# Performance work log

Hardware: AMD Instinct MI355X
Metric: run time of the kernel (lower is better)

Reference implementation:

```python
import jax, jax.numpy as jnp
import numpy as np

UP_FACTOR = 8
POINT_ORDER_WEIGHT = 0.1


def _interp_linear(x, size):
    """torch.nn.functional.interpolate(mode='linear', align_corners=True) on last dim.
    x: (N, C, W) -> (N, C, size)"""
    W = x.shape[-1]
    pos = jnp.linspace(0.0, W - 1.0, size)          # align_corners=True mapping
    i0 = jnp.floor(pos).astype(jnp.int32)
    i1 = jnp.minimum(i0 + 1, W - 1)
    w = (pos - i0.astype(pos.dtype)).astype(x.dtype)
    return x[..., i0] * (1.0 - w) + x[..., i1] * w


def _directed_loss(points1, points2, mask):
    """Chamfer-style directed loss: for each point in points2, min sq-dist to points1,
    plus index-order penalty on the argmin indices. points*: (N, 2, W')."""
    # pairwise sq distances: d[n, i, j] = sum_c (points2[n,c,i] - points1[n,c,j])^2
    d = jnp.square(points2[:, :, :, None] - points1[:, :, None, :]).sum(axis=1)  # (N, W', W')
    mse_error = d.min(axis=2)                         # (N, W')
    indices = d.argmin(axis=2)                        # (N, W') int
    neg_index_diffs = -(indices[:, 1:] - indices[:, :-1]).astype(jnp.float32)
    neg_index_diffs = jnp.square(jax.nn.relu(neg_index_diffs))
    mse_error = mse_error * mask
    neg_index_diffs = neg_index_diffs * mask[:, :-1]
    return mse_error.mean() + (POINT_ORDER_WEIGHT * neg_index_diffs).mean()


def setup_inputs() -> dict:
    key = jax.random.key(0)
    k1, k2, k3 = jax.random.split(key, 3)
    N, C, W = 128, 2, 128
    return {
        "target_points": jax.random.normal(k1, (N, C, W), dtype=jnp.float32),
        "predictions": jax.random.normal(k2, (N, C, W), dtype=jnp.float32),
        "visibility_mask": jax.random.uniform(k3, (N, W), dtype=jnp.float32),
    }


def reference(target_points, predictions, visibility_mask):
    size = target_points.shape[2] * UP_FACTOR  # compared_size = W * up_factor
    t = _interp_linear(target_points, size)    # (N, 2, W')
    p = _interp_linear(predictions, size)      # (N, 2, W')
    m = _interp_linear(visibility_mask[:, None, :], size)[:, 0, :]  # (N, W')
    m = jnp.where(m < 0.5, jnp.zeros_like(m), m)

    # direct (aligned) error
    error_direct = (jnp.square(t - p).sum(axis=1) * m).mean(axis=1)  # (N,)

    # symmetric matched (chamfer + index-order) error
    error_matched = 0.5 * _directed_loss(p, t, m) + 0.5 * _directed_loss(t, p, m)

    return jnp.minimum(error_matched, error_direct.mean())
```

## Files before the change

kernel.cpp:

```cpp
#include <hip/hip_runtime.h>

#define N_BATCH 128
#define W_RAW   128
#define NSEG    (W_RAW - 1)
#define W_UP    1024
#define TPB     256
#define QCHUNK  4
#define QPB     256
#define SCHUNK  4
#define SPC     32
#define NBLK    (N_BATCH * 2 * QCHUNK)

#define WS_S 0
#define WS_P 1024
#define WS_D 2048
#define WS_I 3072

__device__ __forceinline__ void interp_setup(int i, int& i0, int& i1, float& w, float& w0) {
    const double step = 127.0 / 1023.0;
    double pos = (double)i * step;
    i0 = (int)pos;
    if (i0 > W_RAW - 1) i0 = W_RAW - 1;
    i1 = min(i0 + 1, W_RAW - 1);
    w  = (float)(pos - (double)i0);
    w0 = __fsub_rn(1.0f, w);
}

__global__ __launch_bounds__(TPB) void chamfer_kernel(
    const float* __restrict__ tp,
    const float* __restrict__ pr,
    const float* __restrict__ vm,
    float* __restrict__ ws)
{
    __shared__ float2 s_c[W_UP];
    __shared__ float4 s_segA[NSEG];
    __shared__ float2 s_segB[NSEG];
    __shared__ float  s_pd[SCHUNK][QPB];
    __shared__ int    s_pi[SCHUNK][QPB];
    __shared__ float  s_red[4 * 3];

    const int bid    = blockIdx.x;
    const int qchunk = bid & (QCHUNK - 1);
    const int dir    = (bid >> 2) & 1;
    const int n      = bid >> 3;
    const int tid    = threadIdx.x;
    const int nd     = n * 2 + dir;

    const float* q_base = (dir == 0) ? tp : pr;
    const float* c_base = (dir == 0) ? pr : tp;
    const float* qx_raw = q_base + (size_t)(n * 2 + 0) * W_RAW;
    const float* qy_raw = q_base + (size_t)(n * 2 + 1) * W_RAW;
    const float* cx_raw = c_base + (size_t)(n * 2 + 0) * W_RAW;
    const float* cy_raw = c_base + (size_t)(n * 2 + 1) * W_RAW;
    const float* m_raw  = vm + (size_t)n * W_RAW;

    #pragma unroll
    for (int k = 0; k < W_UP / TPB; ++k) {
        const int i = tid + k * TPB;
        int i0, i1; float w, w0;
        interp_setup(i, i0, i1, w, w0);
        const float cx = __fadd_rn(__fmul_rn(cx_raw[i0], w0), __fmul_rn(cx_raw[i1], w));
        const float cy = __fadd_rn(__fmul_rn(cy_raw[i0], w0), __fmul_rn(cy_raw[i1], w));
        s_c[i] = make_float2(cx, cy);
    }

    if (tid < NSEG) {
        const int s = tid;
        const float ax = cx_raw[s],     ay = cy_raw[s];
        const float bx = cx_raw[s + 1], by = cy_raw[s + 1];
        const float abx = bx - ax, aby = by - ay;
        const float len2 = abx * abx + aby * aby;
        const float inv  = (len2 > 0.0f) ? (1.0f / len2) : 0.0f;
        const float Kx = abx * inv, Ky = aby * inv;
        const float bb = -(ax * abx + ay * aby) * inv;
        const float s8h = (float)s * (1023.0f / 127.0f) + 0.5f;
        s_segA[s] = make_float4(Kx, Ky, bb, s8h);
        s_segB[s] = make_float2((float)((s * 1023 + 126) / 127),
                                (float)(((s + 1) * 1023) / 127));
    }

    const int jc = tid >> 6;
    const int g  = tid & 63;

    float qx[4], qy[4];
    #pragma unroll
    for (int k = 0; k < 4; ++k) {
        const int qi = qchunk * QPB + g * 4 + k;
        int i0, i1; float w, w0;
        interp_setup(qi, i0, i1, w, w0);
        qx[k] = __fadd_rn(__fmul_rn(qx_raw[i0], w0), __fmul_rn(qx_raw[i1], w));
        qy[k] = __fadd_rn(__fmul_rn(qy_raw[i0], w0), __fmul_rn(qy_raw[i1], w));
    }
    __syncthreads();

    float bestd[4];
    int   bidx[4];
    #pragma unroll
    for (int k = 0; k < 4; ++k) { bestd[k] = 3.4e38f; bidx[k] = 0; }

    const int sbase = jc * SPC;
    const int send  = min(sbase + SPC, NSEG);
    #pragma unroll 4
    for (int s = sbase; s < send; ++s) {
        const float4 SA = s_segA[s];
        const float2 SB = s_segB[s];
        #pragma unroll
        for (int k = 0; k < 4; ++k) {
            const float t  = __builtin_fmaf(qy[k], SA.y, __builtin_fmaf(qx[k], SA.x, SA.z));
            float ic = __builtin_fmaf(t, 1023.0f / 127.0f, SA.w);
            ic = fminf(fmaxf(ic, SB.x), SB.y);
            const int i0 = (int)ic;
            const float2 c0 = s_c[i0];
            const float dx0 = __fsub_rn(qx[k], c0.x);
            const float dy0 = __fsub_rn(qy[k], c0.y);
            const float d0  = __fadd_rn(__fmul_rn(dx0, dx0), __fmul_rn(dy0, dy0));
            const bool lt = d0 < bestd[k];
            bestd[k] = lt ? d0 : bestd[k];
            bidx[k]  = lt ? i0 : bidx[k];
        }
    }

    #pragma unroll
    for (int k = 0; k < 4; ++k) {
        const int q = g * 4 + k;
        s_pd[jc][q] = bestd[k];
        s_pi[jc][q] = bidx[k];
    }
    __syncthreads();

    float bd = s_pd[0][tid];
    int   bi = s_pi[0][tid];
    #pragma unroll
    for (int c = 1; c < SCHUNK; ++c) {
        const float d2 = s_pd[c][tid];
        const bool lt = d2 < bd;
        bd = lt ? d2 : bd;
        bi = lt ? s_pi[c][tid] : bi;
    }
    s_pi[0][tid] = bi;

    const int qi = qchunk * QPB + tid;
    ((int*)(ws + WS_I))[(size_t)nd * W_UP + qi] = bi;

    int i0m, i1m; float wm, w0m;
    interp_setup(qi, i0m, i1m, wm, w0m);
    const float qxm = __fadd_rn(__fmul_rn(qx_raw[i0m], w0m), __fmul_rn(qx_raw[i1m], wm));
    const float qym = __fadd_rn(__fmul_rn(qy_raw[i0m], w0m), __fmul_rn(qy_raw[i1m], wm));
    const float mv  = __fadd_rn(__fmul_rn(m_raw[i0m], w0m), __fmul_rn(m_raw[i1m], wm));
    const float mq  = (mv < 0.5f) ? 0.0f : mv;

    float S = bd * mq;
    float D = 0.0f;
    if (dir == 0) {
        const float2 c = s_c[qi];
        const float dx = qxm - c.x;
        const float dy = qym - c.y;
        D = (dx * dx + dy * dy) * mq;
    }
    __syncthreads();

    float P = 0.0f;
    if (tid < QPB - 1) {
        const float df = (float)(s_pi[0][tid] - s_pi[0][tid + 1]);
        const float r  = fmaxf(df, 0.0f);
        P = r * r * mq;
    }

    #pragma unroll
    for (int off = 32; off > 0; off >>= 1) {
        S += __shfl_down(S, off, 64);
        P += __shfl_down(P, off, 64);
        D += __shfl_down(D, off, 64);
    }
    const int wave = tid >> 6, lane = tid & 63;
    if (lane == 0) {
        s_red[wave * 3 + 0] = S;
        s_red[wave * 3 + 1] = P;
        s_red[wave * 3 + 2] = D;
    }
    __syncthreads();
    if (tid == 0) {
        float St = 0.f, Pt = 0.f, Dt = 0.f;
        #pragma unroll
        for (int w2 = 0; w2 < TPB / 64; ++w2) {
            St += s_red[w2 * 3 + 0];
            Pt += s_red[w2 * 3 + 1];
            Dt += s_red[w2 * 3 + 2];
        }
        ws[WS_S + bid] = St;
        ws[WS_P + bid] = Pt;
        ws[WS_D + bid] = Dt;
    }
}

__global__ __launch_bounds__(TPB) void finalize_kernel(
    const float* __restrict__ vm,
    const float* __restrict__ ws,
    float* __restrict__ out)
{
    __shared__ float s_red[4 * 3];
    const int tid = threadIdx.x;

    float S = 0.f, P = 0.f, D = 0.f;
    #pragma unroll
    for (int k = 0; k < NBLK / TPB; ++k) {
        const int b = tid + k * TPB;
        S += ws[WS_S + b];
        P += ws[WS_P + b];
        D += ws[WS_D + b];
    }

    if (tid < N_BATCH * 2 * (QCHUNK - 1)) {
        const int nd = tid / (QCHUNK - 1);
        const int b  = tid % (QCHUNK - 1) + 1;
        const int i  = b * QPB - 1;
        const int n  = nd >> 1;
        const int* widx = (const int*)(ws + WS_I) + (size_t)nd * W_UP;
        const float df = (float)(widx[i] - widx[i + 1]);
        const float r  = fmaxf(df, 0.0f);
        int i0, i1; float w, w0;
        interp_setup(i, i0, i1, w, w0);
        const float* m_raw = vm + (size_t)n * W_RAW;
        float mv = __fadd_rn(__fmul_rn(m_raw[i0], w0), __fmul_rn(m_raw[i1], w));
        const float mq = (mv < 0.5f) ? 0.0f : mv;
        P += r * r * mq;
    }

    #pragma unroll
    for (int off = 32; off > 0; off >>= 1) {
        S += __shfl_down(S, off, 64);
        P += __shfl_down(P, off, 64);
        D += __shfl_down(D, off, 64);
    }
    const int wave = tid >> 6, lane = tid & 63;
    if (lane == 0) {
        s_red[wave * 3 + 0] = S;
        s_red[wave * 3 + 1] = P;
        s_red[wave * 3 + 2] = D;
    }
    __syncthreads();
    if (tid == 0) {
        float St = 0.f, Pt = 0.f, Dt = 0.f;
        #pragma unroll
        for (int w2 = 0; w2 < TPB / 64; ++w2) {
            St += s_red[w2 * 3 + 0];
            Pt += s_red[w2 * 3 + 1];
            Dt += s_red[w2 * 3 + 2];
        }
        const float nw  = (float)(N_BATCH * W_UP);
        const float nw1 = (float)(N_BATCH * (W_UP - 1));
        const float matched = St / (2.0f * nw) + 0.1f * Pt / (2.0f * nw1);
        const float direct  = Dt / nw;
        out[0] = fminf(matched, direct);
    }
}

extern "C" void kernel_launch(void* const* d_in, const int* in_sizes, int n_in,
                              void* d_out, int out_size, void* d_ws, size_t ws_size,
                              hipStream_t stream) {
    const float* tp = (const float*)d_in[0];
    const float* pr = (const float*)d_in[1];
    const float* vm = (const float*)d_in[2];
    float* out = (float*)d_out;
    float* ws  = (float*)d_ws;

    chamfer_kernel<<<NBLK, TPB, 0, stream>>>(tp, pr, vm, ws);
    finalize_kernel<<<1, TPB, 0, stream>>>(vm, ws, out);
}
```

Measured before the change: 73.98 us.

## Split queries into 8 chunks per direction and store only chunk boundary indices

Doubles the number of blocks by halving queries per block (128 instead of 256), so each thread handles 2 queries instead of 4, which spreads work over more CUs. Instead of writing all argmin indices to the workspace, each block stores only the first and last index of its chunk, and the finalize kernel now loops over the larger set of chunk boundaries. It also adds a launch-bounds occupancy hint. The trade-off is that every block redundantly rebuilds the upsampled candidate curve and segment tables, and half the threads sit idle during the final per-query reduction.

```diff
diff --git a/kernel.cpp b/kernel.cpp
--- a/kernel.cpp
+++ b/kernel.cpp
@@ -5,16 +5,16 @@
 #define NSEG    (W_RAW - 1)
 #define W_UP    1024
 #define TPB     256
-#define QCHUNK  4
-#define QPB     256
+#define QCHUNK  8
+#define QPB     128
 #define SCHUNK  4
 #define SPC     32
 #define NBLK    (N_BATCH * 2 * QCHUNK)
 
 #define WS_S 0
-#define WS_P 1024
-#define WS_D 2048
-#define WS_I 3072
+#define WS_P NBLK
+#define WS_D (2 * NBLK)
+#define WS_I (3 * NBLK)
 
 __device__ __forceinline__ void interp_setup(int i, int& i0, int& i1, float& w, float& w0) {
     const double step = 127.0 / 1023.0;
@@ -26,7 +26,7 @@
     w0 = __fsub_rn(1.0f, w);
 }
 
-__global__ __launch_bounds__(TPB) void chamfer_kernel(
+__global__ __launch_bounds__(TPB, 8) void chamfer_kernel(
     const float* __restrict__ tp,
     const float* __restrict__ pr,
     const float* __restrict__ vm,
@@ -41,8 +41,8 @@
 
     const int bid    = blockIdx.x;
     const int qchunk = bid & (QCHUNK - 1);
-    const int dir    = (bid >> 2) & 1;
-    const int n      = bid >> 3;
+    const int dir    = (bid >> 3) & 1;
+    const int n      = bid >> 4;
     const int tid    = threadIdx.x;
     const int nd     = n * 2 + dir;
 
@@ -82,10 +82,10 @@
     const int jc = tid >> 6;
     const int g  = tid & 63;
 
-    float qx[4], qy[4];
-    #pragma unroll
-    for (int k = 0; k < 4; ++k) {
-        const int qi = qchunk * QPB + g * 4 + k;
+    float qx[2], qy[2];
+    #pragma unroll
+    for (int k = 0; k < 2; ++k) {
+        const int qi = qchunk * QPB + g * 2 + k;
         int i0, i1; float w, w0;
         interp_setup(qi, i0, i1, w, w0);
         qx[k] = __fadd_rn(__fmul_rn(qx_raw[i0], w0), __fmul_rn(qx_raw[i1], w));
@@ -93,10 +93,10 @@
     }
     __syncthreads();
 
-    float bestd[4];
-    int   bidx[4];
-    #pragma unroll
-    for (int k = 0; k < 4; ++k) { bestd[k] = 3.4e38f; bidx[k] = 0; }
+    float bestd[2];
+    int   bidx[2];
+    #pragma unroll
+    for (int k = 0; k < 2; ++k) { bestd[k] = 3.4e38f; bidx[k] = 0; }
 
     const int sbase = jc * SPC;
     const int send  = min(sbase + SPC, NSEG);
@@ -105,7 +105,7 @@
         const float4 SA = s_segA[s];
         const float2 SB = s_segB[s];
         #pragma unroll
-        for (int k = 0; k < 4; ++k) {
+        for (int k = 0; k < 2; ++k) {
             const float t  = __builtin_fmaf(qy[k], SA.y, __builtin_fmaf(qx[k], SA.x, SA.z));
             float ic = __builtin_fmaf(t, 1023.0f / 127.0f, SA.w);
             ic = fminf(fmaxf(ic, SB.x), SB.y);
@@ -121,45 +121,49 @@
     }
 
     #pragma unroll
-    for (int k = 0; k < 4; ++k) {
-        const int q = g * 4 + k;
+    for (int k = 0; k < 2; ++k) {
+        const int q = g * 2 + k;
         s_pd[jc][q] = bestd[k];
         s_pi[jc][q] = bidx[k];
     }
     __syncthreads();
 
-    float bd = s_pd[0][tid];
-    int   bi = s_pi[0][tid];
-    #pragma unroll
-    for (int c = 1; c < SCHUNK; ++c) {
-        const float d2 = s_pd[c][tid];
-        const bool lt = d2 < bd;
-        bd = lt ? d2 : bd;
-        bi = lt ? s_pi[c][tid] : bi;
-    }
-    s_pi[0][tid] = bi;
-
-    const int qi = qchunk * QPB + tid;
-    ((int*)(ws + WS_I))[(size_t)nd * W_UP + qi] = bi;
-
-    int i0m, i1m; float wm, w0m;
-    interp_setup(qi, i0m, i1m, wm, w0m);
-    const float qxm = __fadd_rn(__fmul_rn(qx_raw[i0m], w0m), __fmul_rn(qx_raw[i1m], wm));
-    const float qym = __fadd_rn(__fmul_rn(qy_raw[i0m], w0m), __fmul_rn(qy_raw[i1m], wm));
-    const float mv  = __fadd_rn(__fmul_rn(m_raw[i0m], w0m), __fmul_rn(m_raw[i1m], wm));
-    const float mq  = (mv < 0.5f) ? 0.0f : mv;
-
-    float S = bd * mq;
-    float D = 0.0f;
-    if (dir == 0) {
-        const float2 c = s_c[qi];
-        const float dx = qxm - c.x;
-        const float dy = qym - c.y;
-        D = (dx * dx + dy * dy) * mq;
-    }
-    __syncthreads();
-
-    float P = 0.0f;
+    float S = 0.0f, P = 0.0f, D = 0.0f;
+    float mq = 0.0f;
+    int   bi = 0;
+    if (tid < QPB) {
+        float bd = s_pd[0][tid];
+        bi = s_pi[0][tid];
+        #pragma unroll
+        for (int c = 1; c < SCHUNK; ++c) {
+            const float d2 = s_pd[c][tid];
+            const bool lt = d2 < bd;
+            bd = lt ? d2 : bd;
+            bi = lt ? s_pi[c][tid] : bi;
+        }
+        s_pi[0][tid] = bi;
+
+        const int qi = qchunk * QPB + tid;
+
+        int i0m, i1m; float wm, w0m;
+        interp_setup(qi, i0m, i1m, wm, w0m);
+        const float qxm = __fadd_rn(__fmul_rn(qx_raw[i0m], w0m), __fmul_rn(qx_raw[i1m], wm));
+        const float qym = __fadd_rn(__fmul_rn(qy_raw[i0m], w0m), __fmul_rn(qy_raw[i1m], wm));
+        const float mv  = __fadd_rn(__fmul_rn(m_raw[i0m], w0m), __fmul_rn(m_raw[i1m], wm));
+        mq = (mv < 0.5f) ? 0.0f : mv;
+
+        S = bd * mq;
+        if (dir == 0) {
+            const float2 c = s_c[qi];
+            const float dx = qxm - c.x;
+            const float dy = qym - c.y;
+            D = (dx * dx + dy * dy) * mq;
+        }
+    }
+    if (tid == 0)       ((int*)(ws + WS_I))[nd * 16 + qchunk * 2 + 0] = bi;
+    if (tid == QPB - 1) ((int*)(ws + WS_I))[nd * 16 + qchunk * 2 + 1] = bi;
+    __syncthreads();
+
     if (tid < QPB - 1) {
         const float df = (float)(s_pi[0][tid] - s_pi[0][tid + 1]);
         const float r  = fmaxf(df, 0.0f);
@@ -210,13 +214,15 @@
         D += ws[WS_D + b];
     }
 
-    if (tid < N_BATCH * 2 * (QCHUNK - 1)) {
-        const int nd = tid / (QCHUNK - 1);
-        const int b  = tid % (QCHUNK - 1) + 1;
+    const int* wsI = (const int*)(ws + WS_I);
+    for (int e = tid; e < N_BATCH * 2 * (QCHUNK - 1); e += TPB) {
+        const int nd = e / (QCHUNK - 1);
+        const int b  = e % (QCHUNK - 1) + 1;
         const int i  = b * QPB - 1;
         const int n  = nd >> 1;
-        const int* widx = (const int*)(ws + WS_I) + (size_t)nd * W_UP;
-        const float df = (float)(widx[i] - widx[i + 1]);
+        const int idx_last  = wsI[nd * 16 + (b - 1) * 2 + 1];
+        const int idx_first = wsI[nd * 16 + b * 2 + 0];
+        const float df = (float)(idx_last - idx_first);
         const float r  = fmaxf(df, 0.0f);
         int i0, i1; float w, w0;
         interp_setup(i, i0, i1, w, w0);
```

Measured after the change: 75.54 us. 1.02x slower.

## Split interpolation and segment setup into a prep kernel, one query per thread

Applied to the files above, without the earlier changes.

Adds a prep kernel that interpolates points and mask once and precomputes per-segment projection coefficients into workspace, replacing the per-block recomputation that was repeated across the four query chunks and two directions. The chamfer kernel now loads those precomputed arrays. Each thread handles one query over all 127 segments, which removes the cross-wave partial-min reduction through shared memory. Only the boundary argmin indices are written out for the finalize step. The cost is an extra kernel launch and global round trip, plus segment data read from global memory with uniform addresses instead of from LDS.

```diff
diff --git a/kernel.cpp b/kernel.cpp
--- a/kernel.cpp
+++ b/kernel.cpp
@@ -7,14 +7,17 @@
 #define TPB     256
 #define QCHUNK  4
 #define QPB     256
-#define SCHUNK  4
-#define SPC     32
 #define NBLK    (N_BATCH * 2 * QCHUNK)
 
-#define WS_S 0
-#define WS_P 1024
-#define WS_D 2048
-#define WS_I 3072
+#define WS_S  0
+#define WS_P  1024
+#define WS_D  2048
+#define WS_I  3072
+#define WS_T  8192
+#define WS_PP (WS_T + 2 * 128 * 1024)
+#define WS_M  (WS_PP + 2 * 128 * 1024)
+#define WS_GA (WS_M + 128 * 1024)
+#define WS_GB (WS_GA + 2 * 128 * NSEG * 4)
 
 __device__ __forceinline__ void interp_setup(int i, int& i0, int& i1, float& w, float& w0) {
     const double step = 127.0 / 1023.0;
@@ -26,17 +29,68 @@
     w0 = __fsub_rn(1.0f, w);
 }
 
-__global__ __launch_bounds__(TPB) void chamfer_kernel(
+__global__ __launch_bounds__(TPB) void prep_kernel(
     const float* __restrict__ tp,
     const float* __restrict__ pr,
     const float* __restrict__ vm,
     float* __restrict__ ws)
 {
+    const int b   = blockIdx.x;
+    const int tid = threadIdx.x;
+
+    if (b < 256) {
+        const int which = b >> 7;
+        const int n     = b & 127;
+        const float* src   = (which == 0) ? tp : pr;
+        const float* x_raw = src + (size_t)(n * 2 + 0) * W_RAW;
+        const float* y_raw = src + (size_t)(n * 2 + 1) * W_RAW;
+        float2* dst = (float2*)(ws + (which == 0 ? WS_T : WS_PP)) + (size_t)n * W_UP;
+
+        #pragma unroll
+        for (int k = 0; k < W_UP / TPB; ++k) {
+            const int i = tid + k * TPB;
+            int i0, i1; float w, w0;
+            interp_setup(i, i0, i1, w, w0);
+            const float cx = __fadd_rn(__fmul_rn(x_raw[i0], w0), __fmul_rn(x_raw[i1], w));
+            const float cy = __fadd_rn(__fmul_rn(y_raw[i0], w0), __fmul_rn(y_raw[i1], w));
+            dst[i] = make_float2(cx, cy);
+        }
+
+        if (tid < NSEG) {
+            const int s = tid;
+            const float ax = x_raw[s],     ay = y_raw[s];
+            const float bx = x_raw[s + 1], by = y_raw[s + 1];
+            const float abx = bx - ax, aby = by - ay;
+            const float len2 = abx * abx + aby * aby;
+            const float inv  = (len2 > 0.0f) ? (1.0f / len2) : 0.0f;
+            const float Kx = abx * inv, Ky = aby * inv;
+            const float bb = -(ax * abx + ay * aby) * inv;
+            const float s8h = (float)s * (1023.0f / 127.0f) + 0.5f;
+            ((float4*)(ws + WS_GA))[(size_t)(which * 128 + n) * NSEG + s] =
+                make_float4(Kx, Ky, bb, s8h);
+            ((float2*)(ws + WS_GB))[(size_t)(which * 128 + n) * NSEG + s] =
+                make_float2((float)((s * 1023 + 126) / 127),
+                            (float)(((s + 1) * 1023) / 127));
+        }
+    } else {
+        const int n = b - 256;
+        const float* m_raw = vm + (size_t)n * W_RAW;
+        float* dst = ws + WS_M + (size_t)n * W_UP;
+        #pragma unroll
+        for (int k = 0; k < W_UP / TPB; ++k) {
+            const int i = tid + k * TPB;
+            int i0, i1; float w, w0;
+            interp_setup(i, i0, i1, w, w0);
+            dst[i] = __fadd_rn(__fmul_rn(m_raw[i0], w0), __fmul_rn(m_raw[i1], w));
+        }
+    }
+}
+
+__global__ __launch_bounds__(TPB) void chamfer_kernel(
+    float* __restrict__ ws)
+{
     __shared__ float2 s_c[W_UP];
-    __shared__ float4 s_segA[NSEG];
-    __shared__ float2 s_segB[NSEG];
-    __shared__ float  s_pd[SCHUNK][QPB];
-    __shared__ int    s_pi[SCHUNK][QPB];
+    __shared__ int    s_pi[QPB];
     __shared__ float  s_red[4 * 3];
 
     const int bid    = blockIdx.x;
@@ -46,122 +100,62 @@
     const int tid    = threadIdx.x;
     const int nd     = n * 2 + dir;
 
-    const float* q_base = (dir == 0) ? tp : pr;
-    const float* c_base = (dir == 0) ? pr : tp;
-    const float* qx_raw = q_base + (size_t)(n * 2 + 0) * W_RAW;
-    const float* qy_raw = q_base + (size_t)(n * 2 + 1) * W_RAW;
-    const float* cx_raw = c_base + (size_t)(n * 2 + 0) * W_RAW;
-    const float* cy_raw = c_base + (size_t)(n * 2 + 1) * W_RAW;
-    const float* m_raw  = vm + (size_t)n * W_RAW;
-
-    #pragma unroll
-    for (int k = 0; k < W_UP / TPB; ++k) {
-        const int i = tid + k * TPB;
-        int i0, i1; float w, w0;
-        interp_setup(i, i0, i1, w, w0);
-        const float cx = __fadd_rn(__fmul_rn(cx_raw[i0], w0), __fmul_rn(cx_raw[i1], w));
-        const float cy = __fadd_rn(__fmul_rn(cy_raw[i0], w0), __fmul_rn(cy_raw[i1], w));
-        s_c[i] = make_float2(cx, cy);
-    }
-
-    if (tid < NSEG) {
-        const int s = tid;
-        const float ax = cx_raw[s],     ay = cy_raw[s];
-        const float bx = cx_raw[s + 1], by = cy_raw[s + 1];
-        const float abx = bx - ax, aby = by - ay;
-        const float len2 = abx * abx + aby * aby;
-        const float inv  = (len2 > 0.0f) ? (1.0f / len2) : 0.0f;
-        const float Kx = abx * inv, Ky = aby * inv;
-        const float bb = -(ax * abx + ay * aby) * inv;
-        const float s8h = (float)s * (1023.0f / 127.0f) + 0.5f;
-        s_segA[s] = make_float4(Kx, Ky, bb, s8h);
-        s_segB[s] = make_float2((float)((s * 1023 + 126) / 127),
-                                (float)(((s + 1) * 1023) / 127));
-    }
-
-    const int jc = tid >> 6;
-    const int g  = tid & 63;
-
-    float qx[4], qy[4];
-    #pragma unroll
-    for (int k = 0; k < 4; ++k) {
-        const int qi = qchunk * QPB + g * 4 + k;
-        int i0, i1; float w, w0;
-        interp_setup(qi, i0, i1, w, w0);
-        qx[k] = __fadd_rn(__fmul_rn(qx_raw[i0], w0), __fmul_rn(qx_raw[i1], w));
-        qy[k] = __fadd_rn(__fmul_rn(qy_raw[i0], w0), __fmul_rn(qy_raw[i1], w));
-    }
-    __syncthreads();
-
-    float bestd[4];
-    int   bidx[4];
-    #pragma unroll
-    for (int k = 0; k < 4; ++k) { bestd[k] = 3.4e38f; bidx[k] = 0; }
-
-    const int sbase = jc * SPC;
-    const int send  = min(sbase + SPC, NSEG);
+    const int cw = (dir == 0) ? 1 : 0;
+    const float2* ccur = (const float2*)(ws + (cw ? WS_PP : WS_T)) + (size_t)n * W_UP;
+    const float2* qcur = (const float2*)(ws + (cw ? WS_T : WS_PP)) + (size_t)n * W_UP;
+    const float4* gA   = (const float4*)(ws + WS_GA) + (size_t)(cw * 128 + n) * NSEG;
+    const float2* gB   = (const float2*)(ws + WS_GB) + (size_t)(cw * 128 + n) * NSEG;
+
+    {
+        const float4* c4  = (const float4*)ccur;
+        float4*       s4  = (float4*)s_c;
+        s4[tid]       = c4[tid];
+        s4[tid + TPB] = c4[tid + TPB];
+    }
+
+    const int qi = qchunk * QPB + tid;
+    const float2 q  = qcur[qi];
+    const float  mv = ws[WS_M + (size_t)n * W_UP + qi];
+    const float  mq = (mv < 0.5f) ? 0.0f : mv;
+    __syncthreads();
+
+    float bd = 3.4e38f;
+    int   bi = 0;
     #pragma unroll 4
-    for (int s = sbase; s < send; ++s) {
-        const float4 SA = s_segA[s];
-        const float2 SB = s_segB[s];
-        #pragma unroll
-        for (int k = 0; k < 4; ++k) {
-            const float t  = __builtin_fmaf(qy[k], SA.y, __builtin_fmaf(qx[k], SA.x, SA.z));
-            float ic = __builtin_fmaf(t, 1023.0f / 127.0f, SA.w);
-            ic = fminf(fmaxf(ic, SB.x), SB.y);
-            const int i0 = (int)ic;
-            const float2 c0 = s_c[i0];
-            const float dx0 = __fsub_rn(qx[k], c0.x);
-            const float dy0 = __fsub_rn(qy[k], c0.y);
-            const float d0  = __fadd_rn(__fmul_rn(dx0, dx0), __fmul_rn(dy0, dy0));
-            const bool lt = d0 < bestd[k];
-            bestd[k] = lt ? d0 : bestd[k];
-            bidx[k]  = lt ? i0 : bidx[k];
-        }
-    }
-
-    #pragma unroll
-    for (int k = 0; k < 4; ++k) {
-        const int q = g * 4 + k;
-        s_pd[jc][q] = bestd[k];
-        s_pi[jc][q] = bidx[k];
-    }
-    __syncthreads();
-
-    float bd = s_pd[0][tid];
-    int   bi = s_pi[0][tid];
-    #pragma unroll
-    for (int c = 1; c < SCHUNK; ++c) {
-        const float d2 = s_pd[c][tid];
-        const bool lt = d2 < bd;
-        bd = lt ? d2 : bd;
-        bi = lt ? s_pi[c][tid] : bi;
-    }
-    s_pi[0][tid] = bi;
-
-    const int qi = qchunk * QPB + tid;
-    ((int*)(ws + WS_I))[(size_t)nd * W_UP + qi] = bi;
-
-    int i0m, i1m; float wm, w0m;
-    interp_setup(qi, i0m, i1m, wm, w0m);
-    const float qxm = __fadd_rn(__fmul_rn(qx_raw[i0m], w0m), __fmul_rn(qx_raw[i1m], wm));
-    const float qym = __fadd_rn(__fmul_rn(qy_raw[i0m], w0m), __fmul_rn(qy_raw[i1m], wm));
-    const float mv  = __fadd_rn(__fmul_rn(m_raw[i0m], w0m), __fmul_rn(m_raw[i1m], wm));
-    const float mq  = (mv < 0.5f) ? 0.0f : mv;
+    for (int s = 0; s < NSEG; ++s) {
+        const float4 SA = gA[s];
+        const float2 SB = gB[s];
+        const float t  = __builtin_fmaf(q.y, SA.y, __builtin_fmaf(q.x, SA.x, SA.z));
+        float ic = __builtin_fmaf(t, 1023.0f / 127.0f, SA.w);
+        ic = fminf(fmaxf(ic, SB.x), SB.y);
+        const int i0 = (int)ic;
+        const float2 c0 = s_c[i0];
+        const float dx0 = __fsub_rn(q.x, c0.x);
+        const float dy0 = __fsub_rn(q.y, c0.y);
+        const float d0  = __fadd_rn(__fmul_rn(dx0, dx0), __fmul_rn(dy0, dy0));
+        const bool lt = d0 < bd;
+        bd = lt ? d0 : bd;
+        bi = lt ? i0 : bi;
+    }
+
+    s_pi[tid] = bi;
+
+    if (tid == 0)       ((int*)(ws + WS_I))[nd * 8 + qchunk * 2 + 0] = bi;
+    if (tid == QPB - 1) ((int*)(ws + WS_I))[nd * 8 + qchunk * 2 + 1] = bi;
 
     float S = bd * mq;
     float D = 0.0f;
     if (dir == 0) {
         const float2 c = s_c[qi];
-        const float dx = qxm - c.x;
-        const float dy = qym - c.y;
+        const float dx = q.x - c.x;
+        const float dy = q.y - c.y;
         D = (dx * dx + dy * dy) * mq;
     }
     __syncthreads();
 
     float P = 0.0f;
     if (tid < QPB - 1) {
-        const float df = (float)(s_pi[0][tid] - s_pi[0][tid + 1]);
+        const float df = (float)(s_pi[tid] - s_pi[tid + 1]);
         const float r  = fmaxf(df, 0.0f);
         P = r * r * mq;
     }
@@ -194,7 +188,6 @@
 }
 
 __global__ __launch_bounds__(TPB) void finalize_kernel(
-    const float* __restrict__ vm,
     const float* __restrict__ ws,
     float* __restrict__ out)
 {
@@ -210,18 +203,17 @@
         D += ws[WS_D + b];
     }
 
-    if (tid < N_BATCH * 2 * (QCHUNK - 1)) {
-        const int nd = tid / (QCHUNK - 1);
-        const int b  = tid % (QCHUNK - 1) + 1;
-        const int i  = b * QPB - 1;
-        const int n  = nd >> 1;
-        const int* widx = (const int*)(ws + WS_I) + (size_t)nd * W_UP;
-        const float df = (float)(widx[i] - widx[i + 1]);
+    const int* wsI = (const int*)(ws + WS_I);
+    for (int e = tid; e < N_BATCH * 2 * (QCHUNK - 1); e += TPB) {
+        const int ndb = e / (QCHUNK - 1);
+        const int b   = e % (QCHUNK - 1) + 1;
+        const int i   = b * QPB - 1;
+        const int nn  = ndb >> 1;
+        const int idx_last  = wsI[ndb * 8 + (b - 1) * 2 + 1];
+        const int idx_first = wsI[ndb * 8 + b * 2 + 0];
+        const float df = (float)(idx_last - idx_first);
         const float r  = fmaxf(df, 0.0f);
-        int i0, i1; float w, w0;
-        interp_setup(i, i0, i1, w, w0);
-        const float* m_raw = vm + (size_t)n * W_RAW;
-        float mv = __fadd_rn(__fmul_rn(m_raw[i0], w0), __fmul_rn(m_raw[i1], w));
+        const float mv = ws[WS_M + (size_t)nn * W_UP + i];
         const float mq = (mv < 0.5f) ? 0.0f : mv;
         P += r * r * mq;
     }
@@ -264,6 +256,7 @@
     float* out = (float*)d_out;
     float* ws  = (float*)d_ws;
 
-    chamfer_kernel<<<NBLK, TPB, 0, stream>>>(tp, pr, vm, ws);
-    finalize_kernel<<<1, TPB, 0, stream>>>(vm, ws, out);
-}
+    prep_kernel<<<384, TPB, 0, stream>>>(tp, pr, vm, ws);
+    chamfer_kernel<<<NBLK, TPB, 0, stream>>>(ws);
+    finalize_kernel<<<1, TPB, 0, stream>>>(ws, out);
+}
```

Result: slower. 88.28 us (+19.3%).
